# Performance work log

Measured on AMD Instinct MI355X. Metric: run time of the kernel, lower is better.

Reference implementation:

```python
import math
import jax
import jax.numpy as jnp
import numpy as np

IMAGE_SIZE = 256
FOV_DEG = 60.0
NEAR, FAR = 0.01, 10.0
CHUNK = 128          # faces processed per scan step (bounds peak memory)
BIG_Z = 1e10         # 'infinite' depth for empty pixels


def _projection_matrix():
    f = 1.0 / math.tan(math.radians(FOV_DEG) / 2)
    return jnp.array([
        [f, 0.0, 0.0, 0.0],
        [0.0, f, 0.0, 0.0],
        [0.0, 0.0, (FAR + NEAR) / (NEAR - FAR), 2.0 * FAR * NEAR / (NEAR - FAR)],
        [0.0, 0.0, -1.0, 0.0],
    ], dtype=jnp.float32)


def _rasterize_mask(v_ndc, faces):
    """Coverage mask via edge-function triangle rasterization with a z-buffer.
    v_ndc: [V,3] ndc coords, faces: [F,3] int. Returns float [H,W] mask."""
    H = W = IMAGE_SIZE
    dt = v_ndc.dtype
    px = ((jnp.arange(W, dtype=dt) + 0.5) / W * 2.0 - 1.0)[None, None, :]  # [1,1,W]
    py = ((jnp.arange(H, dtype=dt) + 0.5) / H * 2.0 - 1.0)[None, :, None]  # [1,H,1]
    fchunks = faces.reshape(-1, CHUNK, 3)

    def body(carry, fc):
        zbuf, mask = carry
        tri = v_ndc[fc]  # [C,3,3]
        x0 = tri[:, 0, 0][:, None, None]; y0 = tri[:, 0, 1][:, None, None]; z0 = tri[:, 0, 2][:, None, None]
        x1 = tri[:, 1, 0][:, None, None]; y1 = tri[:, 1, 1][:, None, None]; z1 = tri[:, 1, 2][:, None, None]
        x2 = tri[:, 2, 0][:, None, None]; y2 = tri[:, 2, 1][:, None, None]; z2 = tri[:, 2, 2][:, None, None]
        # edge functions, [C,H,W]
        e0 = (x1 - x0) * (py - y0) - (y1 - y0) * (px - x0)
        e1 = (x2 - x1) * (py - y1) - (y2 - y1) * (px - x1)
        e2 = (x0 - x2) * (py - y2) - (y0 - y2) * (px - x2)
        inside = ((e0 >= 0) & (e1 >= 0) & (e2 >= 0)) | ((e0 <= 0) & (e1 <= 0) & (e2 <= 0))
        area = e0 + e1 + e2
        denom = jnp.where(jnp.abs(area) > 1e-12, area, 1.0)
        # barycentric-interpolated depth
        z = (e1 * z0 + e2 * z1 + e0 * z2) / denom
        zc = jnp.where(inside, z, BIG_Z)
        zbuf = jnp.minimum(zbuf, jnp.min(zc, axis=0))
        mask = jnp.maximum(mask, jnp.max(inside.astype(dt), axis=0))
        return (zbuf, mask), None

    zbuf0 = jnp.full((H, W), BIG_Z, dtype=dt)
    mask0 = jnp.zeros((H, W), dtype=dt)
    (_, mask), _ = jax.lax.scan(body, (zbuf0, mask0), fchunks)
    return mask


def setup_inputs() -> dict:
    key = jax.random.key(0)
    k1, k2, k3, k4 = jax.random.split(key, 4)
    B, V, F = 2, 4096, 4096
    verts = jax.random.normal(k1, (B, V, 3), dtype=jnp.float32)
    faces = jax.random.randint(k2, (B, F, 3), 0, V, dtype=jnp.int64 if jax.config.jax_enable_x64 else jnp.int32)
    R = jax.random.normal(k3, (B, 3, 3), dtype=jnp.float32)
    T = jax.random.normal(k4, (B, 3), dtype=jnp.float32)
    return {"verts": verts, "faces": faces, "R": R, "T": T}


def reference(verts, faces, R, T):
    proj = _projection_matrix()
    # world2cam: [R^T | -R^T t] with homogeneous bottom row, built batched
    Rt = jnp.swapaxes(R, -1, -2)                       # [B,3,3]
    t = -jnp.einsum('bij,bj->bi', Rt, T)               # [B,3]
    top = jnp.concatenate([Rt, t[..., None]], axis=-1)  # [B,3,4]
    bottom = jnp.broadcast_to(jnp.array([[0.0, 0.0, 0.0, 1.0]], dtype=verts.dtype), (R.shape[0], 1, 4))
    w2c = jnp.concatenate([top, bottom], axis=1)       # [B,4,4]
    VP = jnp.einsum('ij,bjk->bik', proj, w2c)          # [B,4,4]
    homo = jnp.concatenate([verts, jnp.ones_like(verts[..., :1])], axis=-1)  # [B,V,4]
    cam = jnp.einsum('bvk,bjk->bvj', homo, VP)         # verts_homo @ VP.T
    ndc = cam[..., :3] / jnp.maximum(cam[..., 3:], 1e-8)  # clamp(min=1e-8)
    mask = jax.vmap(_rasterize_mask)(ndc, faces)       # [B,H,W]
    return jnp.repeat(mask[..., None], 3, axis=-1)     # [B,H,W,3]
```

## Files before the change

### kernel.cpp

```cpp
#include <hip/hip_runtime.h>


#pragma clang fp contract(off)

#define HW      256
#define BATCH   2
#define VCOUNT  4096
#define FCOUNT  4096
#define CULL_EPS 1.52587890625e-05f

__global__ __launch_bounds__(256)
void face_pack_kernel(const float* __restrict__ verts,
                      const int* __restrict__ faces,
                      const float* __restrict__ R,
                      const float* __restrict__ T,
                      float4* __restrict__ fxy4,
                      float2* __restrict__ fxy2,
                      float4* __restrict__ ed0,
                      float4* __restrict__ ed1,
                      float4* __restrict__ ed2)
{
#pragma clang fp contract(off)
    int gid = blockIdx.x * blockDim.x + threadIdx.x;
    if (gid >= BATCH * FCOUNT) return;
    int b = gid / FCOUNT;

    const float fproj = 1.7320508075688772f;

    const float* Rb = R + b * 9;
    const float* Tb = T + b * 3;

    float t0 = -((Rb[0*3+0]*Tb[0] + Rb[1*3+0]*Tb[1]) + Rb[2*3+0]*Tb[2]);
    float t1 = -((Rb[0*3+1]*Tb[0] + Rb[1*3+1]*Tb[1]) + Rb[2*3+1]*Tb[2]);
    float t2 = -((Rb[0*3+2]*Tb[0] + Rb[1*3+2]*Tb[1]) + Rb[2*3+2]*Tb[2]);

    float VP00 = fproj * Rb[0*3+0], VP01 = fproj * Rb[1*3+0],
          VP02 = fproj * Rb[2*3+0], VP03 = fproj * t0;
    float VP10 = fproj * Rb[0*3+1], VP11 = fproj * Rb[1*3+1],
          VP12 = fproj * Rb[2*3+1], VP13 = fproj * t1;
    float VP30 = -Rb[0*3+2], VP31 = -Rb[1*3+2],
          VP32 = -Rb[2*3+2], VP33 = -t2;

    const int* fp = faces + (size_t)gid * 3;
    float xs[3], ys[3];
#pragma unroll
    for (int j = 0; j < 3; ++j) {
        const float* vv = verts + ((size_t)b * VCOUNT + fp[j]) * 3;
        float vx = vv[0], vy = vv[1], vz = vv[2];
        float cx = ((vx*VP00 + vy*VP01) + vz*VP02) + VP03;
        float cy = ((vx*VP10 + vy*VP11) + vz*VP12) + VP13;
        float cw = ((vx*VP30 + vy*VP31) + vz*VP32) + VP33;
        float w = fmaxf(cw, 1e-8f);
        xs[j] = cx / w;
        ys[j] = cy / w;
    }

    fxy4[gid] = make_float4(xs[0], ys[0], xs[1], ys[1]);
    fxy2[gid] = make_float2(xs[2], ys[2]);

    float d01x = xs[1] - xs[0], d01y = ys[1] - ys[0];
    float d12x = xs[2] - xs[1], d12y = ys[2] - ys[1];
    float d20x = xs[0] - xs[2], d20y = ys[0] - ys[2];

    float C0 = d01y * xs[0] - d01x * ys[0];
    float C1 = d12y * xs[1] - d12x * ys[1];
    float C2 = d20y * xs[2] - d20x * ys[2];
    float e0r = CULL_EPS * (fabsf(d01x) * (1.0f + fabsf(ys[0]))
                          + fabsf(d01y) * (1.0f + fabsf(xs[0])));
    float e1r = CULL_EPS * (fabsf(d12x) * (1.0f + fabsf(ys[1]))
                          + fabsf(d12y) * (1.0f + fabsf(xs[1])));
    float e2r = CULL_EPS * (fabsf(d20x) * (1.0f + fabsf(ys[2]))
                          + fabsf(d20y) * (1.0f + fabsf(xs[2])));

    ed0[gid] = make_float4(d01x, -d01y, C0, e0r);
    ed1[gid] = make_float4(d12x, -d12y, C1, e1r);
    ed2[gid] = make_float4(d20x, -d20y, C2, e2r);
}

__device__ __forceinline__ float bcast_lane(float v, int k) {
    return __int_as_float(__builtin_amdgcn_readlane(__float_as_int(v), k));
}

__global__ __launch_bounds__(64)
void raster_kernel(const float4* __restrict__ ed0,
                   const float4* __restrict__ ed1,
                   const float4* __restrict__ ed2,
                   const float4* __restrict__ fxy4,
                   const float2* __restrict__ fxy2,
                   float* __restrict__ out)
{
#pragma clang fp contract(off)
    int b    = blockIdx.y;
    int tile = blockIdx.x;
    int qx = (tile & 31) << 3;
    int qy = (tile >> 5) << 3;
    int lane = threadIdx.x;
    int px_i = qx + (lane & 7);
    int py_i = qy + (lane >> 3);

    float px = (((float)px_i + 0.5f) / 256.0f) * 2.0f - 1.0f;
    float py = (((float)py_i + 0.5f) / 256.0f) * 2.0f - 1.0f;

    float pxlo = (((float)qx       + 0.5f) / 256.0f) * 2.0f - 1.0f;
    float pxhi = (((float)(qx + 7) + 0.5f) / 256.0f) * 2.0f - 1.0f;
    float pylo = (((float)qy       + 0.5f) / 256.0f) * 2.0f - 1.0f;
    float pyhi = (((float)(qy + 7) + 0.5f) / 256.0f) * 2.0f - 1.0f;
    float xm = 0.5f * (pxlo + pxhi), xr = 0.5f * (pxhi - pxlo);
    float ym = 0.5f * (pylo + pyhi), yr = 0.5f * (pyhi - pylo);

    const float4* e0p = ed0  + (size_t)b * FCOUNT;
    const float4* e1p = ed1  + (size_t)b * FCOUNT;
    const float4* e2p = ed2  + (size_t)b * FCOUNT;
    const float4* f4  = fxy4 + (size_t)b * FCOUNT;
    const float2* f2  = fxy2 + (size_t)b * FCOUNT;

    bool covered = false;

    for (int g = 0; g < FCOUNT; g += 64) {
        if (__all((int)covered)) break;

        int idx = g + lane;
        float4 E0 = e0p[idx];
        float4 E1 = e1p[idx];
        float4 E2 = e2p[idx];
        float4 q0 = f4[idx];
        float2 q1 = f2[idx];

        bool killneg = false, killpos = false;
        {
#pragma clang fp contract(fast)
            float b0 = E0.x * ym + E0.y * xm + E0.z;
            float s0 = fabsf(E0.x) * yr + fabsf(E0.y) * xr;
            killneg = killneg || (b0 + s0 < -E0.w);
            killpos = killpos || (b0 - s0 >  E0.w);
            float b1 = E1.x * ym + E1.y * xm + E1.z;
            float s1 = fabsf(E1.x) * yr + fabsf(E1.y) * xr;
            killneg = killneg || (b1 + s1 < -E1.w);
            killpos = killpos || (b1 - s1 >  E1.w);
            float b2 = E2.x * ym + E2.y * xm + E2.z;
            float s2 = fabsf(E2.x) * yr + fabsf(E2.y) * xr;
            killneg = killneg || (b2 + s2 < -E2.w);
            killpos = killpos || (b2 - s2 >  E2.w);
        }
        bool skip = killneg && killpos;

        unsigned long long m = __ballot((int)!skip);
        while (m) {
            int k = __ffsll((long long)m) - 1;
            m &= m - 1;
            float A0 = bcast_lane(E0.x, k), B0 = bcast_lane(E0.y, k);
            float A1 = bcast_lane(E1.x, k), B1 = bcast_lane(E1.y, k);
            float A2 = bcast_lane(E2.x, k), B2 = bcast_lane(E2.y, k);
            float ax0 = bcast_lane(q0.x, k), ay0 = bcast_lane(q0.y, k);
            float ax1 = bcast_lane(q0.z, k), ay1 = bcast_lane(q0.w, k);
            float ax2 = bcast_lane(q1.x, k), ay2 = bcast_lane(q1.y, k);
            float e0 = A0 * (py - ay0) + B0 * (px - ax0);
            float e1 = A1 * (py - ay1) + B1 * (px - ax1);
            float e2 = A2 * (py - ay2) + B2 * (px - ax2);
            float mn = fminf(fminf(e0, e1), e2);
            float mx = fmaxf(fmaxf(e0, e1), e2);
            covered = covered || (mn >= 0.0f) || (mx <= 0.0f);
        }
    }

    float val = covered ? 1.0f : 0.0f;
    size_t o = ((size_t)(b * HW + py_i) * HW + px_i) * 3;
    out[o + 0] = val;
    out[o + 1] = val;
    out[o + 2] = val;
}

extern "C" void kernel_launch(void* const* d_in, const int* in_sizes, int n_in,
                              void* d_out, int out_size, void* d_ws, size_t ws_size,
                              hipStream_t stream) {
    const float* verts = (const float*)d_in[0];
    const int*   faces = (const int*)d_in[1];
    const float* R     = (const float*)d_in[2];
    const float* T     = (const float*)d_in[3];
    float*       out   = (float*)d_out;

    float4* fxy4 = (float4*)d_ws;
    float2* fxy2 = (float2*)(fxy4 + BATCH * FCOUNT);
    float4* ed0  = (float4*)(fxy2 + BATCH * FCOUNT);
    float4* ed1  = ed0 + BATCH * FCOUNT;
    float4* ed2  = ed1 + BATCH * FCOUNT;

    int nf = BATCH * FCOUNT;
    face_pack_kernel<<<(nf + 255) / 256, 256, 0, stream>>>(verts, faces, R, T,
                                                           fxy4, fxy2,
                                                           ed0, ed1, ed2);

    dim3 grid(32 * 32, BATCH);
    raster_kernel<<<grid, 64, 0, stream>>>(ed0, ed1, ed2, fxy4, fxy2, out);
}
```

Baseline: 63.92 us.

## Split face loop across 8 waves per tile with shared coverage early-exit

Each 8x8 pixel tile now runs 8 wavefronts per block instead of one. Each wave scans a strided subset of face groups, and the waves share per-pixel coverage bitmasks through LDS so all of them can stop once every pixel is covered. This targets the long serial face loop of tiles that have few or no covered pixels, where one wave previously had to walk all 4096 faces. In exchange, covered tiles may do more total work because waves exit independently, and each face group now adds LDS traffic and ballots.

Result: slower. 73.40 us (+14.8%).

```diff
diff --git a/kernel.cpp b/kernel.cpp
--- a/kernel.cpp
+++ b/kernel.cpp
@@ -7,6 +7,7 @@
 #define BATCH   2
 #define VCOUNT  4096
 #define FCOUNT  4096
+#define WAVES   8
 #define CULL_EPS 1.52587890625e-05f
 
 __global__ __launch_bounds__(256)
@@ -81,7 +82,7 @@
     return __int_as_float(__builtin_amdgcn_readlane(__float_as_int(v), k));
 }
 
-__global__ __launch_bounds__(64)
+__global__ __launch_bounds__(64 * WAVES)
 void raster_kernel(const float4* __restrict__ ed0,
                    const float4* __restrict__ ed1,
                    const float4* __restrict__ ed2,
@@ -94,7 +95,8 @@
     int tile = blockIdx.x;
     int qx = (tile & 31) << 3;
     int qy = (tile >> 5) << 3;
-    int lane = threadIdx.x;
+    int wave = threadIdx.x >> 6;
+    int lane = threadIdx.x & 63;
     int px_i = qx + (lane & 7);
     int py_i = qy + (lane >> 3);
 
@@ -114,12 +116,15 @@
     const float4* f4  = fxy4 + (size_t)b * FCOUNT;
     const float2* f2  = fxy2 + (size_t)b * FCOUNT;
 
+    __shared__ unsigned long long wmask[WAVES];
+    if (threadIdx.x < WAVES) wmask[threadIdx.x] = 0ull;
+    __syncthreads();
+    volatile unsigned long long* vm = wmask;
+
     bool covered = false;
 
-    for (int g = 0; g < FCOUNT; g += 64) {
-        if (__all((int)covered)) break;
-
-        int idx = g + lane;
+    for (int g = wave; g < FCOUNT / 64; g += WAVES) {
+        int idx = (g << 6) + lane;
         float4 E0 = e0p[idx];
         float4 E1 = e1p[idx];
         float4 E2 = e2p[idx];
@@ -161,13 +166,28 @@
             float mx = fmaxf(fmaxf(e0, e1), e2);
             covered = covered || (mn >= 0.0f) || (mx <= 0.0f);
         }
+
+        unsigned long long bal = __ballot((int)covered);
+        if (lane == 0) vm[wave] = bal;
+        unsigned long long cur = 0ull;
+#pragma unroll
+        for (int w2 = 0; w2 < WAVES; ++w2) cur |= vm[w2];
+        covered = covered || (((cur >> lane) & 1ull) != 0ull);
+        if (__all((int)covered)) break;
     }
 
-    float val = covered ? 1.0f : 0.0f;
-    size_t o = ((size_t)(b * HW + py_i) * HW + px_i) * 3;
-    out[o + 0] = val;
-    out[o + 1] = val;
-    out[o + 2] = val;
+    __syncthreads();
+
+    if (wave == 0) {
+        unsigned long long fin = 0ull;
+#pragma unroll
+        for (int w2 = 0; w2 < WAVES; ++w2) fin |= wmask[w2];
+        float val = (((fin >> lane) & 1ull) != 0ull) ? 1.0f : 0.0f;
+        size_t o = ((size_t)(b * HW + py_i) * HW + px_i) * 3;
+        out[o + 0] = val;
+        out[o + 1] = val;
+        out[o + 2] = val;
+    }
 }
 
 extern "C" void kernel_launch(void* const* d_in, const int* in_sizes, int n_in,
@@ -191,5 +211,5 @@
                                                            ed0, ed1, ed2);
 
     dim3 grid(32 * 32, BATCH);
-    raster_kernel<<<grid, 64, 0, stream>>>(ed0, ed1, ed2, fxy4, fxy2, out);
-}
+    raster_kernel<<<grid, 64 * WAVES, 0, stream>>>(ed0, ed1, ed2, fxy4, fxy2, out);
+}
```

## Split rasterization into a quick pass plus a multi-wave pass over unresolved tiles

Applied to the files above, without the earlier changes.

Rasterization now runs in three stages. A single-wave pass scans the first few face groups for every tile and records a coverage bitmask. Tiles that are not fully covered are appended to a worklist with an atomic counter, and an 8-wave block per listed tile then splits the remaining face groups across waves, merging coverage with atomicOr and exiting early once the shared mask is full. A final kernel expands the bitmasks into the output image. The aim is to spread long-tail tiles (uncovered background that must scan every face) across more waves, at the cost of two extra launches, atomics and a grid of mostly idle blocks in the second pass.

Result: slower. 68.96 us (+7.9%).

```diff
diff --git a/kernel.cpp b/kernel.cpp
--- a/kernel.cpp
+++ b/kernel.cpp
@@ -7,6 +7,9 @@
 #define BATCH   2
 #define VCOUNT  4096
 #define FCOUNT  4096
+#define NTILES  1024
+#define GTILES  (BATCH * NTILES)
+#define K_CAP   8
 #define CULL_EPS 1.52587890625e-05f
 
 __global__ __launch_bounds__(256)
@@ -18,10 +21,12 @@
                       float2* __restrict__ fxy2,
                       float4* __restrict__ ed0,
                       float4* __restrict__ ed1,
-                      float4* __restrict__ ed2)
+                      float4* __restrict__ ed2,
+                      unsigned* __restrict__ count)
 {
 #pragma clang fp contract(off)
     int gid = blockIdx.x * blockDim.x + threadIdx.x;
+    if (gid == 0) *count = 0u;
     if (gid >= BATCH * FCOUNT) return;
     int b = gid / FCOUNT;
 
@@ -81,13 +86,64 @@
     return __int_as_float(__builtin_amdgcn_readlane(__float_as_int(v), k));
 }
 
+__device__ __forceinline__ void scan_group(
+    int idx,
+    const float4* __restrict__ e0p, const float4* __restrict__ e1p,
+    const float4* __restrict__ e2p, const float4* __restrict__ f4,
+    const float2* __restrict__ f2,
+    float px, float py, float xm, float xr, float ym, float yr,
+    bool& covered)
+{
+    float4 E0 = e0p[idx];
+    float4 E1 = e1p[idx];
+    float4 E2 = e2p[idx];
+    float4 q0 = f4[idx];
+    float2 q1 = f2[idx];
+
+    bool killneg = false, killpos = false;
+    {
+#pragma clang fp contract(fast)
+        float b0 = E0.x * ym + E0.y * xm + E0.z;
+        float s0 = fabsf(E0.x) * yr + fabsf(E0.y) * xr;
+        killneg = killneg || (b0 + s0 < -E0.w);
+        killpos = killpos || (b0 - s0 >  E0.w);
+        float b1 = E1.x * ym + E1.y * xm + E1.z;
+        float s1 = fabsf(E1.x) * yr + fabsf(E1.y) * xr;
+        killneg = killneg || (b1 + s1 < -E1.w);
+        killpos = killpos || (b1 - s1 >  E1.w);
+        float b2 = E2.x * ym + E2.y * xm + E2.z;
+        float s2 = fabsf(E2.x) * yr + fabsf(E2.y) * xr;
+        killneg = killneg || (b2 + s2 < -E2.w);
+        killpos = killpos || (b2 - s2 >  E2.w);
+    }
+    bool skip = killneg && killpos;
+
+    unsigned long long m = __ballot((int)!skip);
+    while (m) {
+        int k = __ffsll((long long)m) - 1;
+        m &= m - 1;
+        float A0 = bcast_lane(E0.x, k), B0 = bcast_lane(E0.y, k);
+        float A1 = bcast_lane(E1.x, k), B1 = bcast_lane(E1.y, k);
+        float A2 = bcast_lane(E2.x, k), B2 = bcast_lane(E2.y, k);
+        float ax0 = bcast_lane(q0.x, k), ay0 = bcast_lane(q0.y, k);
+        float ax1 = bcast_lane(q0.z, k), ay1 = bcast_lane(q0.w, k);
+        float ax2 = bcast_lane(q1.x, k), ay2 = bcast_lane(q1.y, k);
+        float e0 = A0 * (py - ay0) + B0 * (px - ax0);
+        float e1 = A1 * (py - ay1) + B1 * (px - ax1);
+        float e2 = A2 * (py - ay2) + B2 * (px - ax2);
+        float mn = fminf(fminf(e0, e1), e2);
+        float mx = fmaxf(fmaxf(e0, e1), e2);
+        covered = covered || (mn >= 0.0f) || (mx <= 0.0f);
+    }
+}
+
 __global__ __launch_bounds__(64)
-void raster_kernel(const float4* __restrict__ ed0,
-                   const float4* __restrict__ ed1,
-                   const float4* __restrict__ ed2,
-                   const float4* __restrict__ fxy4,
-                   const float2* __restrict__ fxy2,
-                   float* __restrict__ out)
+void raster_a(const float4* __restrict__ ed0, const float4* __restrict__ ed1,
+              const float4* __restrict__ ed2, const float4* __restrict__ fxy4,
+              const float2* __restrict__ fxy2,
+              unsigned* __restrict__ masks,
+              unsigned* __restrict__ list,
+              unsigned* __restrict__ count)
 {
 #pragma clang fp contract(off)
     int b    = blockIdx.y;
@@ -115,56 +171,92 @@
     const float2* f2  = fxy2 + (size_t)b * FCOUNT;
 
     bool covered = false;
-
-    for (int g = 0; g < FCOUNT; g += 64) {
+    for (int g = 0; g < K_CAP * 64; g += 64) {
+        scan_group(g + lane, e0p, e1p, e2p, f4, f2,
+                   px, py, xm, xr, ym, yr, covered);
         if (__all((int)covered)) break;
-
-        int idx = g + lane;
-        float4 E0 = e0p[idx];
-        float4 E1 = e1p[idx];
-        float4 E2 = e2p[idx];
-        float4 q0 = f4[idx];
-        float2 q1 = f2[idx];
-
-        bool killneg = false, killpos = false;
-        {
-#pragma clang fp contract(fast)
-            float b0 = E0.x * ym + E0.y * xm + E0.z;
-            float s0 = fabsf(E0.x) * yr + fabsf(E0.y) * xr;
-            killneg = killneg || (b0 + s0 < -E0.w);
-            killpos = killpos || (b0 - s0 >  E0.w);
-            float b1 = E1.x * ym + E1.y * xm + E1.z;
-            float s1 = fabsf(E1.x) * yr + fabsf(E1.y) * xr;
-            killneg = killneg || (b1 + s1 < -E1.w);
-            killpos = killpos || (b1 - s1 >  E1.w);
-            float b2 = E2.x * ym + E2.y * xm + E2.z;
-            float s2 = fabsf(E2.x) * yr + fabsf(E2.y) * xr;
-            killneg = killneg || (b2 + s2 < -E2.w);
-            killpos = killpos || (b2 - s2 >  E2.w);
+    }
+
+    unsigned long long bal = __ballot((int)covered);
+    int gt = b * NTILES + tile;
+    bool done = (bal == ~0ull);
+    if (lane == 0) {
+        masks[2*gt + 0] = (unsigned)bal;
+        masks[2*gt + 1] = (unsigned)(bal >> 32);
+        if (!done) {
+            unsigned idx = atomicAdd(count, 1u);
+            list[idx] = (unsigned)gt;
         }
-        bool skip = killneg && killpos;
-
-        unsigned long long m = __ballot((int)!skip);
-        while (m) {
-            int k = __ffsll((long long)m) - 1;
-            m &= m - 1;
-            float A0 = bcast_lane(E0.x, k), B0 = bcast_lane(E0.y, k);
-            float A1 = bcast_lane(E1.x, k), B1 = bcast_lane(E1.y, k);
-            float A2 = bcast_lane(E2.x, k), B2 = bcast_lane(E2.y, k);
-            float ax0 = bcast_lane(q0.x, k), ay0 = bcast_lane(q0.y, k);
-            float ax1 = bcast_lane(q0.z, k), ay1 = bcast_lane(q0.w, k);
-            float ax2 = bcast_lane(q1.x, k), ay2 = bcast_lane(q1.y, k);
-            float e0 = A0 * (py - ay0) + B0 * (px - ax0);
-            float e1 = A1 * (py - ay1) + B1 * (px - ax1);
-            float e2 = A2 * (py - ay2) + B2 * (px - ax2);
-            float mn = fminf(fminf(e0, e1), e2);
-            float mx = fmaxf(fmaxf(e0, e1), e2);
-            covered = covered || (mn >= 0.0f) || (mx <= 0.0f);
-        }
-    }
-
-    float val = covered ? 1.0f : 0.0f;
-    size_t o = ((size_t)(b * HW + py_i) * HW + px_i) * 3;
+    }
+}
+
+__global__ __launch_bounds__(512)
+void raster_b(const float4* __restrict__ ed0, const float4* __restrict__ ed1,
+              const float4* __restrict__ ed2, const float4* __restrict__ fxy4,
+              const float2* __restrict__ fxy2,
+              unsigned* __restrict__ masks,
+              const unsigned* __restrict__ list,
+              const unsigned* __restrict__ count)
+{
+#pragma clang fp contract(off)
+    unsigned cnt = *count;
+    if (blockIdx.x >= cnt) return;
+    int gt   = (int)list[blockIdx.x];
+    int b    = gt >> 10;
+    int tile = gt & (NTILES - 1);
+    int wave = threadIdx.x >> 6;
+    int lane = threadIdx.x & 63;
+
+    int qx = (tile & 31) << 3;
+    int qy = (tile >> 5) << 3;
+    int px_i = qx + (lane & 7);
+    int py_i = qy + (lane >> 3);
+
+    float px = (((float)px_i + 0.5f) / 256.0f) * 2.0f - 1.0f;
+    float py = (((float)py_i + 0.5f) / 256.0f) * 2.0f - 1.0f;
+
+    float pxlo = (((float)qx       + 0.5f) / 256.0f) * 2.0f - 1.0f;
+    float pxhi = (((float)(qx + 7) + 0.5f) / 256.0f) * 2.0f - 1.0f;
+    float pylo = (((float)qy       + 0.5f) / 256.0f) * 2.0f - 1.0f;
+    float pyhi = (((float)(qy + 7) + 0.5f) / 256.0f) * 2.0f - 1.0f;
+    float xm = 0.5f * (pxlo + pxhi), xr = 0.5f * (pxhi - pxlo);
+    float ym = 0.5f * (pylo + pyhi), yr = 0.5f * (pyhi - pylo);
+
+    const float4* e0p = ed0  + (size_t)b * FCOUNT;
+    const float4* e1p = ed1  + (size_t)b * FCOUNT;
+    const float4* e2p = ed2  + (size_t)b * FCOUNT;
+    const float4* f4  = fxy4 + (size_t)b * FCOUNT;
+    const float2* f2  = fxy2 + (size_t)b * FCOUNT;
+
+    bool covered = false;
+    for (int gi = K_CAP + wave; gi < FCOUNT / 64; gi += 8) {
+        unsigned lo = masks[2*gt + 0];
+        unsigned hi = masks[2*gt + 1];
+        if ((lo & hi) == 0xffffffffu) break;
+        scan_group((gi << 6) + lane, e0p, e1p, e2p, f4, f2,
+                   px, py, xm, xr, ym, yr, covered);
+    }
+
+    unsigned long long bal = __ballot((int)covered);
+    if (lane == 0) {
+        if ((unsigned)bal)         atomicOr(&masks[2*gt + 0], (unsigned)bal);
+        if ((unsigned)(bal >> 32)) atomicOr(&masks[2*gt + 1], (unsigned)(bal >> 32));
+    }
+}
+
+__global__ __launch_bounds__(256)
+void raster_c(const unsigned* __restrict__ masks, float* __restrict__ out)
+{
+    int gid = blockIdx.x * 256 + threadIdx.x;
+    int b = gid >> 16;
+    int p = gid & 65535;
+    int py = p >> 8, px = p & 255;
+    int tile = ((py >> 3) << 5) + (px >> 3);
+    int gt = b * NTILES + tile;
+    int bit = ((py & 7) << 3) + (px & 7);
+    unsigned word = masks[2*gt + (bit >> 5)];
+    float val = ((word >> (bit & 31)) & 1u) ? 1.0f : 0.0f;
+    size_t o = (size_t)gid * 3;
     out[o + 0] = val;
     out[o + 1] = val;
     out[o + 2] = val;
@@ -184,12 +276,21 @@
     float4* ed0  = (float4*)(fxy2 + BATCH * FCOUNT);
     float4* ed1  = ed0 + BATCH * FCOUNT;
     float4* ed2  = ed1 + BATCH * FCOUNT;
+    unsigned* masks = (unsigned*)(ed2 + BATCH * FCOUNT);
+    unsigned* list  = masks + GTILES * 2;
+    unsigned* count = list + GTILES;
 
     int nf = BATCH * FCOUNT;
     face_pack_kernel<<<(nf + 255) / 256, 256, 0, stream>>>(verts, faces, R, T,
                                                            fxy4, fxy2,
-                                                           ed0, ed1, ed2);
-
-    dim3 grid(32 * 32, BATCH);
-    raster_kernel<<<grid, 64, 0, stream>>>(ed0, ed1, ed2, fxy4, fxy2, out);
-}
+                                                           ed0, ed1, ed2, count);
+
+    dim3 gridA(NTILES, BATCH);
+    raster_a<<<gridA, 64, 0, stream>>>(ed0, ed1, ed2, fxy4, fxy2,
+                                       masks, list, count);
+
+    raster_b<<<GTILES, 512, 0, stream>>>(ed0, ed1, ed2, fxy4, fxy2,
+                                         masks, list, count);
+
+    raster_c<<<(BATCH * HW * HW) / 256, 256, 0, stream>>>(masks, out);
+}
```

## Cull faces against full screen and compact survivors before rasterization

Applied to the files above, without the earlier changes.

The face packing kernel now tests each triangle against the whole-screen bounding box. It drops faces that cannot touch any pixel, and it flags faces that cover the entire screen so every pixel is marked covered at once. Surviving faces are compacted with an atomic counter, and the raster kernel loops only over that count instead of all faces. This adds a memset, global atomics and non-deterministic face order in exchange for fewer per-tile face loads and tests.

Result: slower. 82.25 us (+28.7%).

```diff
diff --git a/kernel.cpp b/kernel.cpp
--- a/kernel.cpp
+++ b/kernel.cpp
@@ -7,6 +7,7 @@
 #define BATCH   2
 #define VCOUNT  4096
 #define FCOUNT  4096
+#define NTILES  1024
 #define CULL_EPS 1.52587890625e-05f
 
 __global__ __launch_bounds__(256)
@@ -18,7 +19,8 @@
                       float2* __restrict__ fxy2,
                       float4* __restrict__ ed0,
                       float4* __restrict__ ed1,
-                      float4* __restrict__ ed2)
+                      float4* __restrict__ ed2,
+                      unsigned* __restrict__ meta)
 {
 #pragma clang fp contract(off)
     int gid = blockIdx.x * blockDim.x + threadIdx.x;
@@ -55,16 +57,13 @@
         ys[j] = cy / w;
     }
 
-    fxy4[gid] = make_float4(xs[0], ys[0], xs[1], ys[1]);
-    fxy2[gid] = make_float2(xs[2], ys[2]);
-
     float d01x = xs[1] - xs[0], d01y = ys[1] - ys[0];
     float d12x = xs[2] - xs[1], d12y = ys[2] - ys[1];
     float d20x = xs[0] - xs[2], d20y = ys[0] - ys[2];
 
-    float C0 = d01y * xs[0] - d01x * ys[0];
-    float C1 = d12y * xs[1] - d12x * ys[1];
-    float C2 = d20y * xs[2] - d20x * ys[2];
+    float A0 = d01x, B0 = -d01y, C0 = d01y * xs[0] - d01x * ys[0];
+    float A1 = d12x, B1 = -d12y, C1 = d12y * xs[1] - d12x * ys[1];
+    float A2 = d20x, B2 = -d20y, C2 = d20y * xs[2] - d20x * ys[2];
     float e0r = CULL_EPS * (fabsf(d01x) * (1.0f + fabsf(ys[0]))
                           + fabsf(d01y) * (1.0f + fabsf(xs[0])));
     float e1r = CULL_EPS * (fabsf(d12x) * (1.0f + fabsf(ys[1]))
@@ -72,9 +71,37 @@
     float e2r = CULL_EPS * (fabsf(d20x) * (1.0f + fabsf(ys[2]))
                           + fabsf(d20y) * (1.0f + fabsf(xs[2])));
 
-    ed0[gid] = make_float4(d01x, -d01y, C0, e0r);
-    ed1[gid] = make_float4(d12x, -d12y, C1, e1r);
-    ed2[gid] = make_float4(d20x, -d20y, C2, e2r);
+    float pxlo = ((0.0f   + 0.5f) / 256.0f) * 2.0f - 1.0f;
+    float pxhi = ((255.0f + 0.5f) / 256.0f) * 2.0f - 1.0f;
+    float xm = 0.5f * (pxlo + pxhi), xr = 0.5f * (pxhi - pxlo);
+    float ym = xm, yr = xr;
+
+    float sb0 = A0 * ym + B0 * xm + C0;
+    float ss0 = fabsf(A0) * yr + fabsf(B0) * xr;
+    float sb1 = A1 * ym + B1 * xm + C1;
+    float ss1 = fabsf(A1) * yr + fabsf(B1) * xr;
+    float sb2 = A2 * ym + B2 * xm + C2;
+    float ss2 = fabsf(A2) * yr + fabsf(B2) * xr;
+    bool cn0 = (sb0 + ss0 < -e0r), cp0 = (sb0 - ss0 > e0r);
+    bool cn1 = (sb1 + ss1 < -e1r), cp1 = (sb1 - ss1 > e1r);
+    bool cn2 = (sb2 + ss2 < -e2r), cp2 = (sb2 - ss2 > e2r);
+
+    bool killneg = cn0 || cn1 || cn2;
+    bool killpos = cp0 || cp1 || cp2;
+    if (killneg && killpos) return;
+
+    if ((cp0 && cp1 && cp2) || (cn0 && cn1 && cn2)) {
+        atomicOr(&meta[2 + b], 1u);
+        return;
+    }
+
+    unsigned ci = atomicAdd(&meta[b], 1u);
+    size_t o = (size_t)b * FCOUNT + ci;
+    fxy4[o] = make_float4(xs[0], ys[0], xs[1], ys[1]);
+    fxy2[o] = make_float2(xs[2], ys[2]);
+    ed0[o] = make_float4(A0, B0, C0, e0r);
+    ed1[o] = make_float4(A1, B1, C1, e1r);
+    ed2[o] = make_float4(A2, B2, C2, e2r);
 }
 
 __device__ __forceinline__ float bcast_lane(float v, int k) {
@@ -87,6 +114,7 @@
                    const float4* __restrict__ ed2,
                    const float4* __restrict__ fxy4,
                    const float2* __restrict__ fxy2,
+                   const unsigned* __restrict__ meta,
                    float* __restrict__ out)
 {
 #pragma clang fp contract(off)
@@ -114,17 +142,20 @@
     const float4* f4  = fxy4 + (size_t)b * FCOUNT;
     const float2* f2  = fxy2 + (size_t)b * FCOUNT;
 
-    bool covered = false;
-
-    for (int g = 0; g < FCOUNT; g += 64) {
+    int cnt = (int)meta[b];
+    bool covered = (meta[2 + b] != 0u);
+
+    for (int g = 0; g < cnt; g += 64) {
         if (__all((int)covered)) break;
 
         int idx = g + lane;
-        float4 E0 = e0p[idx];
-        float4 E1 = e1p[idx];
-        float4 E2 = e2p[idx];
-        float4 q0 = f4[idx];
-        float2 q1 = f2[idx];
+        bool valid = idx < cnt;
+        int li = valid ? idx : (cnt - 1);
+        float4 E0 = e0p[li];
+        float4 E1 = e1p[li];
+        float4 E2 = e2p[li];
+        float4 q0 = f4[li];
+        float2 q1 = f2[li];
 
         bool killneg = false, killpos = false;
         {
@@ -142,7 +173,7 @@
             killneg = killneg || (b2 + s2 < -E2.w);
             killpos = killpos || (b2 - s2 >  E2.w);
         }
-        bool skip = killneg && killpos;
+        bool skip = !valid || (killneg && killpos);
 
         unsigned long long m = __ballot((int)!skip);
         while (m) {
@@ -184,12 +215,15 @@
     float4* ed0  = (float4*)(fxy2 + BATCH * FCOUNT);
     float4* ed1  = ed0 + BATCH * FCOUNT;
     float4* ed2  = ed1 + BATCH * FCOUNT;
+    unsigned* meta = (unsigned*)(ed2 + BATCH * FCOUNT);
+
+    hipMemsetAsync(meta, 0, 4 * sizeof(unsigned), stream);
 
     int nf = BATCH * FCOUNT;
     face_pack_kernel<<<(nf + 255) / 256, 256, 0, stream>>>(verts, faces, R, T,
                                                            fxy4, fxy2,
-                                                           ed0, ed1, ed2);
-
-    dim3 grid(32 * 32, BATCH);
-    raster_kernel<<<grid, 64, 0, stream>>>(ed0, ed1, ed2, fxy4, fxy2, out);
-}
+                                                           ed0, ed1, ed2, meta);
+
+    dim3 grid(NTILES, BATCH);
+    raster_kernel<<<grid, 64, 0, stream>>>(ed0, ed1, ed2, fxy4, fxy2, meta, out);
+}
```
